# Kernel optimization log

Hardware: AMD Instinct MI355X
Metric: run time of the kernel (lower is better)

Reference implementation:

```python
import jax, jax.numpy as jnp
import numpy as np

N, E = 100000, 1600000
F1, H1, H2 = 128, 128, 128


def setup_inputs() -> dict:
    key = jax.random.key(0)
    ks = jax.random.split(key, 8)
    x = jax.random.normal(ks[0], (N, F1), dtype=jnp.float32)
    edge_index = jax.random.randint(ks[1], (2, E), 0, N, dtype=jnp.int64)
    s1 = 1.0 / np.sqrt(F1)
    s2 = 1.0 / np.sqrt(H1)
    s3 = 1.0 / np.sqrt(H2)
    W1 = jax.random.uniform(ks[2], (F1, H1), jnp.float32, -s1, s1)
    b1 = jax.random.uniform(ks[3], (H1,), jnp.float32, -s1, s1)
    W2 = jax.random.uniform(ks[4], (H1, H2), jnp.float32, -s2, s2)
    b2 = jax.random.uniform(ks[5], (H2,), jnp.float32, -s2, s2)
    Wc = jax.random.uniform(ks[6], (H2, 1), jnp.float32, -s3, s3)
    bc = jax.random.uniform(ks[7], (1,), jnp.float32, -s3, s3)
    return {"x": x, "edge_index": edge_index, "W1": W1, "b1": b1,
            "W2": W2, "b2": b2, "Wc": Wc, "bc": bc}


def _gcn_conv(h, W, b, row, col, norm, n):
    # linear transform then degree-normalized gather/scatter-add aggregation
    h = h @ W                                  # [N, out]
    msg = h[row] * norm[:, None]               # [E+N, out] gather + scale
    out = jax.ops.segment_sum(msg, col, num_segments=n)  # scatter-add
    return out + b


def reference(x, edge_index, W1, b1, W2, b2, Wc, bc):
    n = x.shape[0]
    loops = jnp.arange(n, dtype=edge_index.dtype)
    row = jnp.concatenate([edge_index[0], loops])  # sources (with self-loops)
    col = jnp.concatenate([edge_index[1], loops])  # targets (with self-loops)
    deg = jax.ops.segment_sum(jnp.ones_like(col, dtype=x.dtype), col,
                              num_segments=n)
    dinv = jnp.where(deg > 0, jax.lax.rsqrt(deg), 0.0)
    norm = dinv[row] * dinv[col]                   # symmetric normalization

    h = jnp.tanh(_gcn_conv(x, W1, b1, row, col, norm, n))
    h = jnp.tanh(_gcn_conv(h, W2, b2, row, col, norm, n))
    logits = (h @ Wc + bc)[:, 0]                   # [N]
    return jax.nn.softmax(logits)                  # softmax over all nodes
```

## Files before the change

kernel.cpp:

```cpp
#include <hip/hip_runtime.h>
#include <hip/hip_fp16.h>


#define BSHIFT 9
#define BSPAN  512
#define PCHUNK 4096
#define LCAP   12288

typedef _Float16 half8 __attribute__((ext_vector_type(8)));
typedef float floatx4 __attribute__((ext_vector_type(4)));
typedef float floatx2 __attribute__((ext_vector_type(2)));

__device__ inline float tanh_fast(float x) {
    float e = __expf(2.0f * x);
    return 1.0f - 2.0f * __builtin_amdgcn_rcpf(e + 1.0f);
}

__device__ inline void fp8_acc16(floatx2* acc, uint4 v) {
    acc[0] += __builtin_amdgcn_cvt_pk_f32_fp8((int)v.x, false);
    acc[1] += __builtin_amdgcn_cvt_pk_f32_fp8((int)v.x, true);
    acc[2] += __builtin_amdgcn_cvt_pk_f32_fp8((int)v.y, false);
    acc[3] += __builtin_amdgcn_cvt_pk_f32_fp8((int)v.y, true);
    acc[4] += __builtin_amdgcn_cvt_pk_f32_fp8((int)v.z, false);
    acc[5] += __builtin_amdgcn_cvt_pk_f32_fp8((int)v.z, true);
    acc[6] += __builtin_amdgcn_cvt_pk_f32_fp8((int)v.w, false);
    acc[7] += __builtin_amdgcn_cvt_pk_f32_fp8((int)v.w, true);
}

__global__ __launch_bounds__(256) void hist_buckets(const int* __restrict__ col, int E,
                                                    int* __restrict__ bucketCnt) {
    __shared__ int h[256];
    h[threadIdx.x] = 0;
    __syncthreads();
    for (int e = blockIdx.x * 256 + threadIdx.x; e < E; e += gridDim.x * 256)
        atomicAdd(&h[col[e] >> BSHIFT], 1);
    __syncthreads();
    int v = h[threadIdx.x];
    if (v) atomicAdd(&bucketCnt[threadIdx.x], v);
}

__global__ void scan_buckets(const int* __restrict__ cnt, int* __restrict__ bucketPtr,
                             int* __restrict__ cursor, int NB, int E) {
    __shared__ int s[256];
    int t = threadIdx.x;
    int v = (t < NB) ? cnt[t] : 0;
    s[t] = v;
    __syncthreads();
    for (int d = 1; d < 256; d <<= 1) {
        int x = (t >= d) ? s[t - d] : 0;
        __syncthreads();
        s[t] += x;
        __syncthreads();
    }
    if (t < NB) {
        int p = s[t] - v;
        bucketPtr[t] = p;
        cursor[t] = p;
    }
    if (t == 0) bucketPtr[NB] = E;
}

__global__ __launch_bounds__(256) void partition_edges(const int* __restrict__ row,
                                                       const int* __restrict__ col, int E,
                                                       int* __restrict__ cursor,
                                                       unsigned int* __restrict__ pairs) {
    __shared__ int hist[256], sscan[256], gdelta[256], hcur[256];
    __shared__ uint2 stage[PCHUNK];
    int t = threadIdx.x;
    int base = blockIdx.x * PCHUNK;
    int cnt = min(PCHUNK, E - base);
    hist[t] = 0;
    __syncthreads();
    uint2 v[16];
    int b_[16];
#pragma unroll
    for (int k = 0; k < 16; k++) {
        int idx = t + k * 256;
        if (idx < cnt) {
            int c = col[base + idx], r = row[base + idx];
            v[k] = make_uint2((unsigned)c, (unsigned)r);
            b_[k] = c >> BSHIFT;
            atomicAdd(&hist[b_[k]], 1);
        } else b_[k] = -1;
    }
    __syncthreads();
    int hv = hist[t];
    sscan[t] = hv;
    __syncthreads();
    for (int d = 1; d < 256; d <<= 1) {
        int x = (t >= d) ? sscan[t - d] : 0;
        __syncthreads();
        sscan[t] += x;
        __syncthreads();
    }
    int excl = sscan[t] - hv;
    if (hv > 0) {
        int g = atomicAdd(&cursor[t], hv);
        gdelta[t] = g - excl;
    }
    hcur[t] = excl;
    __syncthreads();
#pragma unroll
    for (int k = 0; k < 16; k++) {
        if (b_[k] >= 0) {
            int slot = atomicAdd(&hcur[b_[k]], 1);
            stage[slot] = v[k];
        }
    }
    __syncthreads();
    for (int i = t; i < cnt; i += 256) {
        uint2 p = stage[i];
        pairs[gdelta[p.x >> BSHIFT] + i] = (p.y << BSHIFT) | (p.x & (BSPAN - 1));
    }
}

__global__ __launch_bounds__(256) void build_bucket_csr(const unsigned int* __restrict__ pairs,
                                                        const int* __restrict__ bucketPtr,
                                                        int* __restrict__ rowptr,
                                                        float* __restrict__ dinv,
                                                        int* __restrict__ csr,
                                                        int n, int NB, int E) {
    __shared__ int hist[BSPAN];
    __shared__ int lptr[BSPAN];
    __shared__ int s[256];
    __shared__ int srcStage[LCAP];
    int b = blockIdx.x, t = threadIdx.x;
    int base = bucketPtr[b], cnt = bucketPtr[b + 1] - base;
    int node0 = b << BSHIFT;
    int nn = min(BSPAN, n - node0);
    hist[t] = 0; hist[t + 256] = 0;
    __syncthreads();
    for (int i = t; i < cnt; i += 256)
        atomicAdd(&hist[pairs[base + i] & (BSPAN - 1)], 1);
    __syncthreads();
    int a0 = hist[2 * t], a1 = hist[2 * t + 1];
    int sum = a0 + a1;
    s[t] = sum;
    __syncthreads();
    for (int d = 1; d < 256; d <<= 1) {
        int x = (t >= d) ? s[t - d] : 0;
        __syncthreads();
        s[t] += x;
        __syncthreads();
    }
    int excl = s[t] - sum;
    lptr[2 * t] = excl;
    lptr[2 * t + 1] = excl + a0;
    __syncthreads();
    for (int lc = t; lc < nn; lc += 256) {
        rowptr[node0 + lc] = base + lptr[lc];
        dinv[node0 + lc] = rsqrtf((float)(hist[lc] + 1));
    }
    if (b == NB - 1 && t == 0) rowptr[n] = E;
    __syncthreads();
    hist[t] = 0; hist[t + 256] = 0;
    __syncthreads();
    bool inLds = (cnt <= LCAP);
    for (int i = t; i < cnt; i += 256) {
        unsigned int p = pairs[base + i];
        int lc = p & (BSPAN - 1);
        int rank = atomicAdd(&hist[lc], 1);
        int slot = lptr[lc] + rank;
        if (inLds) srcStage[slot] = (int)(p >> BSHIFT);
        else csr[base + slot] = (int)(p >> BSHIFT);
    }
    __syncthreads();
    if (inLds)
        for (int i = t; i < cnt; i += 256) csr[base + i] = srcStage[i];
}

__global__ __launch_bounds__(256) void prep_wfrags(const float* __restrict__ W1,
                                                   const float* __restrict__ W2,
                                                   uint4* __restrict__ F1,
                                                   uint4* __restrict__ F2) {
    int g = blockIdx.x * 256 + threadIdx.x;
    bool second = (g >= 2048);
    const float* W = second ? W2 : W1;
    uint4* F = second ? F2 : F1;
    int t = g & 2047;
    int lane = t & 63, ct = (t >> 6) & 7, ks = t >> 9;
    int col = ct * 16 + (lane & 15);
    int kb = ks * 32 + (lane >> 4) * 8;
    half8 v;
#pragma unroll
    for (int j = 0; j < 8; j++) {
        int k = kb + j;
        int krow = second ? (((k & 7) << 4) | (k >> 3)) : k;
        v[j] = (_Float16)W[krow * 128 + col];
    }
    F[t] = __builtin_bit_cast(uint4, v);
}

template <bool HALF_IN>
__global__ __launch_bounds__(256) void gemm_mfma(const void* __restrict__ Ap,
                                                 const uint4* __restrict__ F,
                                                 const float* __restrict__ dinv,
                                                 unsigned char* __restrict__ T8, int n) {
    int w = threadIdx.x >> 6, lane = threadIdx.x & 63;
    int r0 = blockIdx.x * 128 + w * 32;
    int rA0 = r0 + (lane & 15);
    int rA1 = rA0 + 16;
    int kc = lane >> 4;
    floatx4 acc[2][8] = {};

#pragma unroll
    for (int ks = 0; ks < 4; ks++) {
        half8 a0 = {}, a1 = {};
        if constexpr (HALF_IN) {
            const uint4* A4 = (const uint4*)Ap;
            if (rA0 < n) a0 = __builtin_bit_cast(half8, A4[(size_t)rA0 * 16 + ks * 4 + kc]);
            if (rA1 < n) a1 = __builtin_bit_cast(half8, A4[(size_t)rA1 * 16 + ks * 4 + kc]);
        } else {
            const float* Af = (const float*)Ap;
            if (rA0 < n) {
                const float4* p = (const float4*)&Af[(size_t)rA0 * 128 + ks * 32 + kc * 8];
                float4 u = p[0], v = p[1];
                a0[0] = (_Float16)u.x; a0[1] = (_Float16)u.y; a0[2] = (_Float16)u.z; a0[3] = (_Float16)u.w;
                a0[4] = (_Float16)v.x; a0[5] = (_Float16)v.y; a0[6] = (_Float16)v.z; a0[7] = (_Float16)v.w;
            }
            if (rA1 < n) {
                const float4* p = (const float4*)&Af[(size_t)rA1 * 128 + ks * 32 + kc * 8];
                float4 u = p[0], v = p[1];
                a1[0] = (_Float16)u.x; a1[1] = (_Float16)u.y; a1[2] = (_Float16)u.z; a1[3] = (_Float16)u.w;
                a1[4] = (_Float16)v.x; a1[5] = (_Float16)v.y; a1[6] = (_Float16)v.z; a1[7] = (_Float16)v.w;
            }
        }
        half8 b[8];
#pragma unroll
        for (int ct = 0; ct < 8; ct++)
            b[ct] = __builtin_bit_cast(half8, F[ks * 512 + ct * 64 + lane]);
#pragma unroll
        for (int ct = 0; ct < 8; ct++) {
            acc[0][ct] = __builtin_amdgcn_mfma_f32_16x16x32_f16(a0, b[ct], acc[0][ct], 0, 0, 0);
            acc[1][ct] = __builtin_amdgcn_mfma_f32_16x16x32_f16(a1, b[ct], acc[1][ct], 0, 0, 0);
        }
    }

    int c = lane & 15;
#pragma unroll
    for (int rt = 0; rt < 2; rt++) {
        int rbase = r0 + rt * 16 + (lane >> 4) * 4;
#pragma unroll
        for (int reg = 0; reg < 4; reg++) {
            int r = rbase + reg;
            if (r < n) {
                float di = dinv[r];
                float vv[8];
#pragma unroll
                for (int ct = 0; ct < 8; ct++) vv[ct] = acc[rt][ct][reg] * di;
                int d0 = __builtin_amdgcn_cvt_pk_fp8_f32(vv[0], vv[1], 0, false);
                d0 = __builtin_amdgcn_cvt_pk_fp8_f32(vv[2], vv[3], d0, true);
                int d1 = __builtin_amdgcn_cvt_pk_fp8_f32(vv[4], vv[5], 0, false);
                d1 = __builtin_amdgcn_cvt_pk_fp8_f32(vv[6], vv[7], d1, true);
                *(uint2*)(T8 + (size_t)r * 128 + c * 8) = make_uint2((unsigned)d0, (unsigned)d1);
            }
        }
    }
}

__global__ __launch_bounds__(256) void aggregate(const unsigned char* __restrict__ T8,
                                                 const int* __restrict__ csr,
                                                 const int* __restrict__ rowptr,
                                                 const float* __restrict__ dinv,
                                                 const float* __restrict__ bias,
                                                 unsigned int* __restrict__ Out, int n) {
    int node = (int)((blockIdx.x * 256 + threadIdx.x) >> 6);
    int lane = threadIdx.x & 63;
    if (node >= n) return;
    int grp = lane >> 3, m = lane & 7;
    const uint4* T4 = (const uint4*)T8;

    floatx2 acc[8] = {};
    int beg = rowptr[node], end = rowptr[node + 1];
    int e = beg;
    while (e < end) {
        int take = min(end - e, 64);
        int myidx = (lane < take) ? csr[e + lane] : 0;
#pragma unroll 2
        for (int j = 0; j < take; j += 8) {
            int src = __shfl(myidx, j + grp);
            if (j + grp < take) fp8_acc16(acc, T4[(size_t)src * 8 + m]);
        }
        e += take;
    }
    float* af = (float*)acc;
#pragma unroll
    for (int q = 0; q < 16; q++) {
        af[q] += __shfl_xor(af[q], 8);
        af[q] += __shfl_xor(af[q], 16);
        af[q] += __shfl_xor(af[q], 32);
    }

    int q = m * 16 + 2 * grp;
    int dim = ((q & 7) << 4) | (q >> 3);
    unsigned short us = *(const unsigned short*)(T8 + (size_t)node * 128 + q);
    floatx2 self = __builtin_amdgcn_cvt_pk_f32_fp8((int)us, false);
    float a0 = acc[grp].x + self.x, a1 = acc[grp].y + self.y;
    float di = dinv[node];
    float b0 = bias[dim], b1 = bias[dim + 16];
    float o0 = tanh_fast(a0 * di + b0);
    float o1 = tanh_fast(a1 * di + b1);
    Out[(size_t)node * 64 + (q >> 1)] =
        __builtin_bit_cast(unsigned int, __floats2half2_rn(o0, o1));
}

__global__ __launch_bounds__(256) void aggregate_logits(const unsigned char* __restrict__ T8,
                                                        const int* __restrict__ csr,
                                                        const int* __restrict__ rowptr,
                                                        const float* __restrict__ dinv,
                                                        const float* __restrict__ bias,
                                                        const float* __restrict__ Wc,
                                                        const float* __restrict__ bc,
                                                        float* __restrict__ logits, int n) {
    int node = (int)((blockIdx.x * 256 + threadIdx.x) >> 6);
    int lane = threadIdx.x & 63;
    if (node >= n) return;
    int grp = lane >> 3, m = lane & 7;
    const uint4* T4 = (const uint4*)T8;

    floatx2 acc[8] = {};
    int beg = rowptr[node], end = rowptr[node + 1];
    int e = beg;
    while (e < end) {
        int take = min(end - e, 64);
        int myidx = (lane < take) ? csr[e + lane] : 0;
#pragma unroll 2
        for (int j = 0; j < take; j += 8) {
            int src = __shfl(myidx, j + grp);
            if (j + grp < take) fp8_acc16(acc, T4[(size_t)src * 8 + m]);
        }
        e += take;
    }
    float* af = (float*)acc;
#pragma unroll
    for (int q = 0; q < 16; q++) {
        af[q] += __shfl_xor(af[q], 8);
        af[q] += __shfl_xor(af[q], 16);
        af[q] += __shfl_xor(af[q], 32);
    }

    int q = m * 16 + 2 * grp;
    int dim = ((q & 7) << 4) | (q >> 3);
    unsigned short us = *(const unsigned short*)(T8 + (size_t)node * 128 + q);
    floatx2 self = __builtin_amdgcn_cvt_pk_f32_fp8((int)us, false);
    float a0 = acc[grp].x + self.x, a1 = acc[grp].y + self.y;
    float di = dinv[node];
    float b0 = bias[dim], b1 = bias[dim + 16];
    float w0 = Wc[dim], w1 = Wc[dim + 16];
    float d = tanh_fast(a0 * di + b0) * w0 + tanh_fast(a1 * di + b1) * w1;
#pragma unroll
    for (int off = 1; off < 64; off <<= 1) d += __shfl_xor(d, off);
    if (lane == 0) logits[node] = d + bc[0];
}

__global__ __launch_bounds__(256) void maxpart(const float* __restrict__ logits, int n,
                                               float* __restrict__ partialMax,
                                               float* __restrict__ denom) {
    if (blockIdx.x == 0 && threadIdx.x == 0) *denom = 0.0f;
    __shared__ float s[256];
    float m = -3.4e38f;
    for (int i = blockIdx.x * 256 + threadIdx.x; i < n; i += 256 * 256)
        m = fmaxf(m, logits[i]);
    s[threadIdx.x] = m;
    __syncthreads();
    for (int d = 128; d; d >>= 1) {
        if (threadIdx.x < d) s[threadIdx.x] = fmaxf(s[threadIdx.x], s[threadIdx.x + d]);
        __syncthreads();
    }
    if (threadIdx.x == 0) partialMax[blockIdx.x] = s[0];
}

__global__ __launch_bounds__(256) void exp_kernel(const float* __restrict__ logits,
                                                  const float* __restrict__ partialMax,
                                                  float* __restrict__ outv,
                                                  float* __restrict__ denom, int n) {
    __shared__ float s[256];
    s[threadIdx.x] = partialMax[threadIdx.x];
    __syncthreads();
    for (int d = 128; d; d >>= 1) {
        if (threadIdx.x < d) s[threadIdx.x] = fmaxf(s[threadIdx.x], s[threadIdx.x + d]);
        __syncthreads();
    }
    float maxv = s[0];
    __syncthreads();
    int i = blockIdx.x * 256 + threadIdx.x;
    float e = 0.0f;
    if (i < n) {
        e = expf(logits[i] - maxv);
        outv[i] = e;
    }
    s[threadIdx.x] = e;
    __syncthreads();
    for (int d = 128; d; d >>= 1) {
        if (threadIdx.x < d) s[threadIdx.x] += s[threadIdx.x + d];
        __syncthreads();
    }
    if (threadIdx.x == 0) atomicAdd(denom, s[0]);
}

__global__ __launch_bounds__(256) void norm_kernel(float* __restrict__ out,
                                                   const float* __restrict__ denom, int n) {
    int i = blockIdx.x * 256 + threadIdx.x;
    if (i < n) out[i] = out[i] / (*denom);
}

extern "C" void kernel_launch(void* const* d_in, const int* in_sizes, int n_in,
                              void* d_out, int out_size, void* d_ws, size_t ws_size,
                              hipStream_t stream) {
    const float* x  = (const float*)d_in[0];
    const int*   ei = (const int*)d_in[1];
    const float* W1 = (const float*)d_in[2];
    const float* b1 = (const float*)d_in[3];
    const float* W2 = (const float*)d_in[4];
    const float* b2 = (const float*)d_in[5];
    const float* Wc = (const float*)d_in[6];
    const float* bc = (const float*)d_in[7];

    int n = in_sizes[0] / 128;
    int E = in_sizes[1] / 2;
    const int* row = ei;
    const int* col = ei + E;
    int NB = (n + BSPAN - 1) >> BSHIFT;

    char* ws = (char*)d_ws;
    size_t off = 0;
    auto alloc = [&](size_t bytes) -> void* {
        void* p = ws + off;
        off += (bytes + 255) & ~(size_t)255;
        return p;
    };
    unsigned char* T1 = (unsigned char*)alloc((size_t)n * 128);
    unsigned char* T2 = (unsigned char*)alloc((size_t)n * 128);
    unsigned int*  H1 = (unsigned int*)alloc((size_t)n * 128 * 2);
    unsigned int* pairs = (unsigned int*)alloc((size_t)E * 4);
    int*    csr      = (int*)alloc((size_t)E * 4);
    float*  dinv     = (float*)alloc((size_t)n * 4);
    int*    rowptr   = (int*)alloc((size_t)(n + 1) * 4);
    int*    bucketCnt= (int*)alloc(256 * 4);
    int*    bucketPtr= (int*)alloc(257 * 4);
    int*    cursor   = (int*)alloc(256 * 4);
    uint4*  F1       = (uint4*)alloc(2048 * 16);
    uint4*  F2       = (uint4*)alloc(2048 * 16);
    float*  logits   = (float*)alloc((size_t)n * 4);
    float*  pmax     = (float*)alloc(256 * 4);
    float*  denom    = (float*)alloc(4);

    int nbN = (n + 255) / 256;
    int nbW = (n + 3) / 4;
    int nbG = (n + 127) / 128;

    hipMemsetAsync(bucketCnt, 0, 256 * 4, stream);

    hist_buckets<<<512, 256, 0, stream>>>(col, E, bucketCnt);
    scan_buckets<<<1, 256, 0, stream>>>(bucketCnt, bucketPtr, cursor, NB, E);
    partition_edges<<<(E + PCHUNK - 1) / PCHUNK, 256, 0, stream>>>(row, col, E, cursor, pairs);
    prep_wfrags<<<16, 256, 0, stream>>>(W1, W2, F1, F2);
    build_bucket_csr<<<NB, 256, 0, stream>>>(pairs, bucketPtr, rowptr, dinv, csr, n, NB, E);

    gemm_mfma<false><<<nbG, 256, 0, stream>>>(x, F1, dinv, T1, n);
    aggregate<<<nbW, 256, 0, stream>>>(T1, csr, rowptr, dinv, b1, H1, n);
    gemm_mfma<true><<<nbG, 256, 0, stream>>>(H1, F2, dinv, T2, n);
    aggregate_logits<<<nbW, 256, 0, stream>>>(T2, csr, rowptr, dinv, b2, Wc, bc, logits, n);

    maxpart<<<256, 256, 0, stream>>>(logits, n, pmax, denom);
    exp_kernel<<<nbN, 256, 0, stream>>>(logits, pmax, (float*)d_out, denom, n);
    norm_kernel<<<nbN, 256, 0, stream>>>((float*)d_out, denom, n);
}
```

Baseline: 235.0 us.

## Pad CSR rows to multiples of four with self-loop and dummy zero row

The CSR build now places each node's self-loop inside its row and pads every row to a multiple of four, filling the padding with an index that points to an extra zero row appended to T1 and T2. The aggregation kernels then run without per-edge bounds checks. Each row is handled by 4 groups of 16 lanes loading 8 bytes each, instead of 8 groups of 8 lanes loading 16 bytes, which also removes one shuffle-reduction stage and the separate self-feature load. The cost is extra padded gathers per row, a larger CSR buffer, and a new small kernel that zeroes the dummy rows.

Result: faster. 218.5 us (-7.0%).

```diff
diff --git a/kernel.cpp b/kernel.cpp
--- a/kernel.cpp
+++ b/kernel.cpp
@@ -6,6 +6,7 @@
 #define BSPAN  512
 #define PCHUNK 4096
 #define LCAP   12288
+#define BPAD   2048
 
 typedef _Float16 half8 __attribute__((ext_vector_type(8)));
 typedef float floatx4 __attribute__((ext_vector_type(4)));
@@ -16,15 +17,11 @@
     return 1.0f - 2.0f * __builtin_amdgcn_rcpf(e + 1.0f);
 }
 
-__device__ inline void fp8_acc16(floatx2* acc, uint4 v) {
+__device__ inline void fp8_acc8(floatx2* acc, uint2 v) {
     acc[0] += __builtin_amdgcn_cvt_pk_f32_fp8((int)v.x, false);
     acc[1] += __builtin_amdgcn_cvt_pk_f32_fp8((int)v.x, true);
     acc[2] += __builtin_amdgcn_cvt_pk_f32_fp8((int)v.y, false);
     acc[3] += __builtin_amdgcn_cvt_pk_f32_fp8((int)v.y, true);
-    acc[4] += __builtin_amdgcn_cvt_pk_f32_fp8((int)v.z, false);
-    acc[5] += __builtin_amdgcn_cvt_pk_f32_fp8((int)v.z, true);
-    acc[6] += __builtin_amdgcn_cvt_pk_f32_fp8((int)v.w, false);
-    acc[7] += __builtin_amdgcn_cvt_pk_f32_fp8((int)v.w, true);
 }
 
 __global__ __launch_bounds__(256) void hist_buckets(const int* __restrict__ col, int E,
@@ -116,16 +113,19 @@
 
 __global__ __launch_bounds__(256) void build_bucket_csr(const unsigned int* __restrict__ pairs,
                                                         const int* __restrict__ bucketPtr,
-                                                        int* __restrict__ rowptr,
+                                                        int* __restrict__ rowptrP,
+                                                        int* __restrict__ rowEndP,
                                                         float* __restrict__ dinv,
-                                                        int* __restrict__ csr,
+                                                        int* __restrict__ csrP,
                                                         int n, int NB, int E) {
     __shared__ int hist[BSPAN];
     __shared__ int lptr[BSPAN];
     __shared__ int s[256];
     __shared__ int srcStage[LCAP];
+    __shared__ int totp;
     int b = blockIdx.x, t = threadIdx.x;
     int base = bucketPtr[b], cnt = bucketPtr[b + 1] - base;
+    int baseP = base + b * BPAD;
     int node0 = b << BSHIFT;
     int nn = min(BSPAN, n - node0);
     hist[t] = 0; hist[t + 256] = 0;
@@ -133,8 +133,9 @@
     for (int i = t; i < cnt; i += 256)
         atomicAdd(&hist[pairs[base + i] & (BSPAN - 1)], 1);
     __syncthreads();
-    int a0 = hist[2 * t], a1 = hist[2 * t + 1];
-    int sum = a0 + a1;
+    int d0 = (2 * t < nn)     ? ((hist[2 * t] + 4) & ~3)     : 0;
+    int d1 = (2 * t + 1 < nn) ? ((hist[2 * t + 1] + 4) & ~3) : 0;
+    int sum = d0 + d1;
     s[t] = sum;
     __syncthreads();
     for (int d = 1; d < 256; d <<= 1) {
@@ -145,28 +146,53 @@
     }
     int excl = s[t] - sum;
     lptr[2 * t] = excl;
-    lptr[2 * t + 1] = excl + a0;
-    __syncthreads();
+    lptr[2 * t + 1] = excl + d0;
+    if (t == 255) totp = s[255];
+    __syncthreads();
+    int cntp = totp;
     for (int lc = t; lc < nn; lc += 256) {
-        rowptr[node0 + lc] = base + lptr[lc];
+        int st = baseP + lptr[lc];
+        int dP = (hist[lc] + 4) & ~3;
+        rowptrP[node0 + lc] = st;
+        rowEndP[node0 + lc] = st + dP;
         dinv[node0 + lc] = rsqrtf((float)(hist[lc] + 1));
     }
-    if (b == NB - 1 && t == 0) rowptr[n] = E;
-    __syncthreads();
-    hist[t] = 0; hist[t + 256] = 0;
-    __syncthreads();
-    bool inLds = (cnt <= LCAP);
-    for (int i = t; i < cnt; i += 256) {
-        unsigned int p = pairs[base + i];
-        int lc = p & (BSPAN - 1);
-        int rank = atomicAdd(&hist[lc], 1);
-        int slot = lptr[lc] + rank;
-        if (inLds) srcStage[slot] = (int)(p >> BSHIFT);
-        else csr[base + slot] = (int)(p >> BSHIFT);
-    }
-    __syncthreads();
-    if (inLds)
-        for (int i = t; i < cnt; i += 256) csr[base + i] = srcStage[i];
+    __syncthreads();
+    bool inLds = (cntp <= LCAP);
+    if (inLds) {
+        for (int i = t; i < cntp; i += 256) srcStage[i] = n;
+        __syncthreads();
+        for (int lc = t; lc < nn; lc += 256) srcStage[lptr[lc]] = node0 + lc;
+        hist[t] = 1; hist[t + 256] = 1;
+        __syncthreads();
+        for (int i = t; i < cnt; i += 256) {
+            unsigned int p = pairs[base + i];
+            int lc = p & (BSPAN - 1);
+            int rank = atomicAdd(&hist[lc], 1);
+            srcStage[lptr[lc] + rank] = (int)(p >> BSHIFT);
+        }
+        __syncthreads();
+        for (int i = t; i < cntp; i += 256) csrP[baseP + i] = srcStage[i];
+    } else {
+        for (int i = t; i < cntp; i += 256) csrP[baseP + i] = n;
+        __syncthreads();
+        for (int lc = t; lc < nn; lc += 256) csrP[baseP + lptr[lc]] = node0 + lc;
+        hist[t] = 1; hist[t + 256] = 1;
+        __syncthreads();
+        for (int i = t; i < cnt; i += 256) {
+            unsigned int p = pairs[base + i];
+            int lc = p & (BSPAN - 1);
+            int rank = atomicAdd(&hist[lc], 1);
+            csrP[baseP + lptr[lc] + rank] = (int)(p >> BSHIFT);
+        }
+    }
+}
+
+__global__ void zero_rows(unsigned char* T1, unsigned char* T2, int n) {
+    int t = threadIdx.x;
+    uint4 z = make_uint4(0, 0, 0, 0);
+    if (t < 8) ((uint4*)(T1 + (size_t)n * 128))[t] = z;
+    else if (t < 16) ((uint4*)(T2 + (size_t)n * 128))[t - 8] = z;
 }
 
 __global__ __launch_bounds__(256) void prep_wfrags(const float* __restrict__ W1,
@@ -259,54 +285,51 @@
 }
 
 __global__ __launch_bounds__(256) void aggregate(const unsigned char* __restrict__ T8,
-                                                 const int* __restrict__ csr,
-                                                 const int* __restrict__ rowptr,
+                                                 const int* __restrict__ csrP,
+                                                 const int* __restrict__ rowptrP,
+                                                 const int* __restrict__ rowEndP,
                                                  const float* __restrict__ dinv,
                                                  const float* __restrict__ bias,
                                                  unsigned int* __restrict__ Out, int n) {
     int node = (int)((blockIdx.x * 256 + threadIdx.x) >> 6);
     int lane = threadIdx.x & 63;
     if (node >= n) return;
-    int grp = lane >> 3, m = lane & 7;
-    const uint4* T4 = (const uint4*)T8;
-
-    floatx2 acc[8] = {};
-    int beg = rowptr[node], end = rowptr[node + 1];
-    int e = beg;
+    int grp = lane >> 4, m = lane & 15;
+    unsigned mo = (unsigned)m << 3;
+
+    floatx2 acc[4] = {};
+    int e = rowptrP[node], end = rowEndP[node];
     while (e < end) {
         int take = min(end - e, 64);
-        int myidx = (lane < take) ? csr[e + lane] : 0;
-#pragma unroll 2
-        for (int j = 0; j < take; j += 8) {
+        int myidx = csrP[e + lane];
+#pragma unroll 4
+        for (int j = 0; j < take; j += 4) {
             int src = __shfl(myidx, j + grp);
-            if (j + grp < take) fp8_acc16(acc, T4[(size_t)src * 8 + m]);
+            uint2 v = *(const uint2*)(T8 + (((unsigned)src << 7) | mo));
+            fp8_acc8(acc, v);
         }
         e += take;
     }
     float* af = (float*)acc;
 #pragma unroll
-    for (int q = 0; q < 16; q++) {
-        af[q] += __shfl_xor(af[q], 8);
+    for (int q = 0; q < 8; q++) {
         af[q] += __shfl_xor(af[q], 16);
         af[q] += __shfl_xor(af[q], 32);
     }
 
-    int q = m * 16 + 2 * grp;
-    int dim = ((q & 7) << 4) | (q >> 3);
-    unsigned short us = *(const unsigned short*)(T8 + (size_t)node * 128 + q);
-    floatx2 self = __builtin_amdgcn_cvt_pk_f32_fp8((int)us, false);
-    float a0 = acc[grp].x + self.x, a1 = acc[grp].y + self.y;
+    floatx2 a = acc[grp];
+    int dim = (grp << 5) | m;
     float di = dinv[node];
-    float b0 = bias[dim], b1 = bias[dim + 16];
-    float o0 = tanh_fast(a0 * di + b0);
-    float o1 = tanh_fast(a1 * di + b1);
-    Out[(size_t)node * 64 + (q >> 1)] =
+    float o0 = tanh_fast(a.x * di + bias[dim]);
+    float o1 = tanh_fast(a.y * di + bias[dim + 16]);
+    Out[(size_t)node * 64 + m * 4 + grp] =
         __builtin_bit_cast(unsigned int, __floats2half2_rn(o0, o1));
 }
 
 __global__ __launch_bounds__(256) void aggregate_logits(const unsigned char* __restrict__ T8,
-                                                        const int* __restrict__ csr,
-                                                        const int* __restrict__ rowptr,
+                                                        const int* __restrict__ csrP,
+                                                        const int* __restrict__ rowptrP,
+                                                        const int* __restrict__ rowEndP,
                                                         const float* __restrict__ dinv,
                                                         const float* __restrict__ bias,
                                                         const float* __restrict__ Wc,
@@ -315,39 +338,34 @@
     int node = (int)((blockIdx.x * 256 + threadIdx.x) >> 6);
     int lane = threadIdx.x & 63;
     if (node >= n) return;
-    int grp = lane >> 3, m = lane & 7;
-    const uint4* T4 = (const uint4*)T8;
-
-    floatx2 acc[8] = {};
-    int beg = rowptr[node], end = rowptr[node + 1];
-    int e = beg;
+    int grp = lane >> 4, m = lane & 15;
+    unsigned mo = (unsigned)m << 3;
+
+    floatx2 acc[4] = {};
+    int e = rowptrP[node], end = rowEndP[node];
     while (e < end) {
         int take = min(end - e, 64);
-        int myidx = (lane < take) ? csr[e + lane] : 0;
-#pragma unroll 2
-        for (int j = 0; j < take; j += 8) {
+        int myidx = csrP[e + lane];
+#pragma unroll 4
+        for (int j = 0; j < take; j += 4) {
             int src = __shfl(myidx, j + grp);
-            if (j + grp < take) fp8_acc16(acc, T4[(size_t)src * 8 + m]);
+            uint2 v = *(const uint2*)(T8 + (((unsigned)src << 7) | mo));
+            fp8_acc8(acc, v);
         }
         e += take;
     }
     float* af = (float*)acc;
 #pragma unroll
-    for (int q = 0; q < 16; q++) {
-        af[q] += __shfl_xor(af[q], 8);
+    for (int q = 0; q < 8; q++) {
         af[q] += __shfl_xor(af[q], 16);
         af[q] += __shfl_xor(af[q], 32);
     }
 
-    int q = m * 16 + 2 * grp;
-    int dim = ((q & 7) << 4) | (q >> 3);
-    unsigned short us = *(const unsigned short*)(T8 + (size_t)node * 128 + q);
-    floatx2 self = __builtin_amdgcn_cvt_pk_f32_fp8((int)us, false);
-    float a0 = acc[grp].x + self.x, a1 = acc[grp].y + self.y;
+    floatx2 a = acc[grp];
+    int dim = (grp << 5) | m;
     float di = dinv[node];
-    float b0 = bias[dim], b1 = bias[dim + 16];
-    float w0 = Wc[dim], w1 = Wc[dim + 16];
-    float d = tanh_fast(a0 * di + b0) * w0 + tanh_fast(a1 * di + b1) * w1;
+    float d = tanh_fast(a.x * di + bias[dim]) * Wc[dim]
+            + tanh_fast(a.y * di + bias[dim + 16]) * Wc[dim + 16];
 #pragma unroll
     for (int off = 1; off < 64; off <<= 1) d += __shfl_xor(d, off);
     if (lane == 0) logits[node] = d + bc[0];
@@ -429,13 +447,14 @@
         off += (bytes + 255) & ~(size_t)255;
         return p;
     };
-    unsigned char* T1 = (unsigned char*)alloc((size_t)n * 128);
-    unsigned char* T2 = (unsigned char*)alloc((size_t)n * 128);
+    unsigned char* T1 = (unsigned char*)alloc((size_t)(n + 1) * 128);
+    unsigned char* T2 = (unsigned char*)alloc((size_t)(n + 1) * 128);
     unsigned int*  H1 = (unsigned int*)alloc((size_t)n * 128 * 2);
+    int*    csrP     = (int*)alloc(((size_t)E + (size_t)NB * BPAD + 64) * 4);
     unsigned int* pairs = (unsigned int*)alloc((size_t)E * 4);
-    int*    csr      = (int*)alloc((size_t)E * 4);
     float*  dinv     = (float*)alloc((size_t)n * 4);
-    int*    rowptr   = (int*)alloc((size_t)(n + 1) * 4);
+    int*    rowptrP  = (int*)alloc((size_t)(n + 1) * 4);
+    int*    rowEndP  = (int*)alloc((size_t)n * 4);
     int*    bucketCnt= (int*)alloc(256 * 4);
     int*    bucketPtr= (int*)alloc(257 * 4);
     int*    cursor   = (int*)alloc(256 * 4);
@@ -455,12 +474,15 @@
     scan_buckets<<<1, 256, 0, stream>>>(bucketCnt, bucketPtr, cursor, NB, E);
     partition_edges<<<(E + PCHUNK - 1) / PCHUNK, 256, 0, stream>>>(row, col, E, cursor, pairs);
     prep_wfrags<<<16, 256, 0, stream>>>(W1, W2, F1, F2);
-    build_bucket_csr<<<NB, 256, 0, stream>>>(pairs, bucketPtr, rowptr, dinv, csr, n, NB, E);
+    build_bucket_csr<<<NB, 256, 0, stream>>>(pairs, bucketPtr, rowptrP, rowEndP, dinv,
+                                             csrP, n, NB, E);
+    zero_rows<<<1, 64, 0, stream>>>(T1, T2, n);
 
     gemm_mfma<false><<<nbG, 256, 0, stream>>>(x, F1, dinv, T1, n);
-    aggregate<<<nbW, 256, 0, stream>>>(T1, csr, rowptr, dinv, b1, H1, n);
+    aggregate<<<nbW, 256, 0, stream>>>(T1, csrP, rowptrP, rowEndP, dinv, b1, H1, n);
     gemm_mfma<true><<<nbG, 256, 0, stream>>>(H1, F2, dinv, T2, n);
-    aggregate_logits<<<nbW, 256, 0, stream>>>(T2, csr, rowptr, dinv, b2, Wc, bc, logits, n);
+    aggregate_logits<<<nbW, 256, 0, stream>>>(T2, csrP, rowptrP, rowEndP, dinv, b2, Wc, bc,
+                                              logits, n);
 
     maxpart<<<256, 256, 0, stream>>>(logits, n, pmax, denom);
     exp_kernel<<<nbN, 256, 0, stream>>>(logits, pmax, (float*)d_out, denom, n);
```
